# Optimization experiments

Hardware: AMD Instinct MI355X
Metric: run time of the kernel (lower is better)

The kernel has to match this reference:

```python
import jax, jax.numpy as jnp
import numpy as np

N = 50000      # num_nodes
E = 800000     # num_edges
D = 128        # node feature dim
ED = 64        # edge feature dim
H = 4          # num_heads
U = 32         # units per head (units*heads == 128)


def setup_inputs() -> dict:
    key = jax.random.key(0)
    ks = jax.random.split(key, 12)
    inputs = jax.random.normal(ks[0], (N, D), dtype=jnp.float32)
    # tf.math.segment_* requires sorted segment ids -> sort source row
    src = jnp.sort(jax.random.randint(ks[1], (E,), 0, N, dtype=jnp.int32))
    dst = jax.random.randint(ks[2], (E,), 0, N, dtype=jnp.int32)
    edge_index = jnp.stack([src, dst], axis=0)
    edge_features = jax.random.normal(ks[3], (E, ED), dtype=jnp.float32)
    def glorot(k, shape):
        lim = np.sqrt(6.0 / (shape[0] + shape[1]))
        return jax.random.uniform(k, shape, jnp.float32, -lim, lim)
    HU = H * U
    return {
        "inputs": inputs,
        "edge_index": edge_index,
        "edge_features": edge_features,
        "Wq": glorot(ks[4], (D, HU)), "bq": jnp.zeros((HU,), jnp.float32),
        "Wk": glorot(ks[5], (D, HU)), "bk": jnp.zeros((HU,), jnp.float32),
        "Wv": glorot(ks[6], (D, HU)), "bv": jnp.zeros((HU,), jnp.float32),
        "We": glorot(ks[7], (ED, HU)), "be": jnp.zeros((HU,), jnp.float32),
        "Wo": glorot(ks[8], (HU, U)), "bo": jnp.zeros((U,), jnp.float32),
    }


def _segment_softmax(scores, seg, num_segments):
    # numerically stable segmented softmax over ragged neighborhoods
    seg_max = jax.ops.segment_max(scores, seg, num_segments=num_segments)
    ex = jnp.exp(scores - seg_max[seg])
    seg_sum = jax.ops.segment_sum(ex, seg, num_segments=num_segments)
    return ex / seg_sum[seg]


def reference(inputs, edge_index, edge_features, Wq, bq, Wk, bk, Wv, bv, We, be, Wo, bo):
    n = inputs.shape[0]
    q = (inputs @ Wq + bq).reshape(n, H, U)
    k = (inputs @ Wk + bk).reshape(n, H, U)
    v = (inputs @ Wv + bv).reshape(n, H, U)
    src, dst = edge_index[0], edge_index[1]
    qi = q[src]                      # [E, H, U]
    kj = k[dst]                      # [E, H, U]
    scores = jnp.sum(qi * kj, axis=-1)   # [E, H]
    eh = (edge_features @ We + be).reshape(-1, H, U)
    scores = scores + jnp.sum(eh * kj, axis=-1)
    attn = _segment_softmax(scores, src, n)        # [E, H]
    attended = jax.ops.segment_sum(attn[..., None] * v[dst], src, num_segments=n)
    attended = attended.reshape(n, H * U)
    return jax.nn.relu(attended @ Wo + bo)
```

## Files before the change

kernel.cpp:

```cpp
#include <hip/hip_runtime.h>
#include <math.h>

#define N_NODES 50000
#define N_EDGES 800000
#define D_IN    128
#define ED_IN   64
#define HU      128
#define NH      4
#define UD      32

#define NPB 16

typedef float fx4 __attribute__((ext_vector_type(4)));
typedef short s16x8 __attribute__((ext_vector_type(8)));
typedef float f32x4 __attribute__((ext_vector_type(4)));

static __device__ __forceinline__ unsigned short f2bf(float f) {
  unsigned u = __float_as_uint(f);
  unsigned r = (u + 0x7FFFu + ((u >> 16) & 1u)) >> 16;
  return (unsigned short)r;
}
static __device__ __forceinline__ float bf_lo(unsigned u) {
  return __uint_as_float(u << 16);
}
static __device__ __forceinline__ float bf_hi(unsigned u) {
  return __uint_as_float(u & 0xFFFF0000u);
}
static __device__ __forceinline__ float dot8(float4 a0, float4 a1, uint4 kk) {
  return a0.x * bf_lo(kk.x) + a0.y * bf_hi(kk.x)
       + a0.z * bf_lo(kk.y) + a0.w * bf_hi(kk.y)
       + a1.x * bf_lo(kk.z) + a1.y * bf_hi(kk.z)
       + a1.z * bf_lo(kk.w) + a1.w * bf_hi(kk.w);
}
static __device__ __forceinline__ float4 f4add(float4 a, float4 b) {
  return make_float4(a.x + b.x, a.y + b.y, a.z + b.z, a.w + b.w);
}

__global__ __launch_bounds__(256) void offsets_kernel(
    const int* __restrict__ src, int* __restrict__ off) {
  const int e = blockIdx.x * 256 + threadIdx.x;
  if (e >= N_EDGES) return;
  const int s = src[e];
  const int prev = (e == 0) ? -1 : src[e - 1];
  for (int n = prev + 1; n <= s; ++n) off[n] = e;
  if (e == N_EDGES - 1)
    for (int n = s + 1; n <= N_NODES; ++n) off[n] = N_EDGES;
}

__global__ __launch_bounds__(256) void wepack_kernel(
    const float* __restrict__ We, unsigned short* __restrict__ wf) {
  const int fl = blockIdx.x * 256 + threadIdx.x;
  if (fl >= 16 * 64) return;
  const int f = fl >> 6, lane = fl & 63;
  const int nt = f >> 1, kh = f & 1;
  const int n = nt * 16 + (lane & 15);
  const int kbase = kh * 32 + (lane >> 4) * 8;
#pragma unroll
  for (int j = 0; j < 8; ++j)
    wf[fl * 8 + j] = f2bf(We[(kbase + j) * HU + n]);
}

__global__ __launch_bounds__(128) void qkv_kernel(
    const float* __restrict__ x,
    const float* __restrict__ Wq, const float* __restrict__ bq,
    const float* __restrict__ Wk, const float* __restrict__ bk,
    const float* __restrict__ Wv, const float* __restrict__ bv,
    const float* __restrict__ be,
    float* __restrict__ q, unsigned short* __restrict__ kbf,
    unsigned short* __restrict__ vbf) {
  const int base = blockIdx.x * NPB;
  const int t = threadIdx.x;
  __shared__ float xs[NPB][D_IN];
  for (int j = 0; j < NPB; ++j)
    xs[j][t] = x[(long)(base + j) * D_IN + t];
  __syncthreads();
  float aq[NPB], ak[NPB], av[NPB];
  const float bqt = bq[t] + be[t], bkt = bk[t], bvt = bv[t];
#pragma unroll
  for (int j = 0; j < NPB; ++j) { aq[j] = bqt; ak[j] = bkt; av[j] = bvt; }
  for (int i = 0; i < D_IN; ++i) {
    const float wq = Wq[i * HU + t];
    const float wk = Wk[i * HU + t];
    const float wv = Wv[i * HU + t];
#pragma unroll
    for (int j = 0; j < NPB; ++j) {
      const float xi = xs[j][i];
      aq[j] += xi * wq; ak[j] += xi * wk; av[j] += xi * wv;
    }
  }
#pragma unroll
  for (int j = 0; j < NPB; ++j) {
    const long nn = base + j;
    q[nn * HU + t] = aq[j];
    kbf[nn * HU + t] = f2bf(ak[j]);
    vbf[nn * HU + t] = f2bf(av[j]);
  }
}

__global__ __launch_bounds__(256) void score_kernel(
    const float* __restrict__ ef,
    const int* __restrict__ src, const int* __restrict__ dst,
    const float* __restrict__ q, const unsigned short* __restrict__ kbf,
    const s16x8* __restrict__ wf,
    float* __restrict__ scores) {
  __shared__ __align__(16) float ehs[4][16 * 64];
  const int t = threadIdx.x;
  const int w = t >> 6, l = t & 63;
  const long ebase = (long)blockIdx.x * 64;
  const int e = (int)(ebase + w * 16 + (l >> 2));
  const int s = src[e], d = dst[e];

  const int arow = (int)(ebase + w * 16 + (l & 15));
  const fx4* ap = (const fx4*)(ef + (long)arow * ED_IN + (l >> 4) * 8);
  const fx4 a00 = __builtin_nontemporal_load(ap);
  const fx4 a01 = __builtin_nontemporal_load(ap + 1);
  const fx4 a10 = __builtin_nontemporal_load(ap + 8);
  const fx4 a11 = __builtin_nontemporal_load(ap + 9);
  s16x8 A0, A1;
  A0[0] = (short)f2bf(a00[0]); A0[1] = (short)f2bf(a00[1]);
  A0[2] = (short)f2bf(a00[2]); A0[3] = (short)f2bf(a00[3]);
  A0[4] = (short)f2bf(a01[0]); A0[5] = (short)f2bf(a01[1]);
  A0[6] = (short)f2bf(a01[2]); A0[7] = (short)f2bf(a01[3]);
  A1[0] = (short)f2bf(a10[0]); A1[1] = (short)f2bf(a10[1]);
  A1[2] = (short)f2bf(a10[2]); A1[3] = (short)f2bf(a10[3]);
  A1[4] = (short)f2bf(a11[0]); A1[5] = (short)f2bf(a11[1]);
  A1[6] = (short)f2bf(a11[2]); A1[7] = (short)f2bf(a11[3]);

  float* __restrict__ ehw = ehs[w];
  const int nb = l & 15, gbase = (l >> 4) * 4;
  const int rloc = l >> 2;
  const int hl = (l >> 1) & 1, half = l & 1;
  const int swzr = (rloc & 7) << 4;

#pragma unroll
  for (int ph = 0; ph < 2; ++ph) {
    f32x4 acc[4];
#pragma unroll
    for (int ntl = 0; ntl < 4; ++ntl) acc[ntl] = (f32x4){0.f, 0.f, 0.f, 0.f};
#pragma unroll
    for (int ntl = 0; ntl < 4; ++ntl) {
      const int f = (ph * 4 + ntl) * 2;
      const s16x8 B0 = wf[(f + 0) * 64 + l];
      const s16x8 B1 = wf[(f + 1) * 64 + l];
      acc[ntl] = __builtin_amdgcn_mfma_f32_16x16x32_bf16(A0, B0, acc[ntl], 0, 0, 0);
      acc[ntl] = __builtin_amdgcn_mfma_f32_16x16x32_bf16(A1, B1, acc[ntl], 0, 0, 0);
    }

#pragma unroll
    for (int ntl = 0; ntl < 4; ++ntl) {
#pragma unroll
      for (int r = 0; r < 4; ++r) {
        const int m = gbase + r;
        const int b = (ntl * 16 + nb) * 4;
        ehw[(m * 256 + (b ^ ((m & 7) << 4))) >> 2] = acc[ntl][r];
      }
    }
    asm volatile("s_waitcnt lgkmcnt(0)" ::: "memory");
    __builtin_amdgcn_sched_barrier(0);

    const int h = ph * 2 + hl;
    const char* ehp = (const char*)(ehw + rloc * 64);
    const int cb = (l & 3) * 64;
    const float4 e0 = *(const float4*)(ehp + ((cb + 0)  ^ swzr));
    const float4 e1 = *(const float4*)(ehp + ((cb + 16) ^ swzr));
    const float4 e2 = *(const float4*)(ehp + ((cb + 32) ^ swzr));
    const float4 e3 = *(const float4*)(ehp + ((cb + 48) ^ swzr));

    const float4* qp = (const float4*)(q + (long)s * HU + h * 32 + half * 16);
    const float4 q0 = qp[0], q1 = qp[1], q2 = qp[2], q3 = qp[3];
    const uint4* kp = (const uint4*)((const char*)kbf + (long)d * 256 + h * 64 + half * 32);
    const uint4 k0 = kp[0], k1 = kp[1];

    float p = dot8(f4add(q0, e0), f4add(q1, e1), k0)
            + dot8(f4add(q2, e2), f4add(q3, e3), k1);
    p += __shfl_xor(p, 1, 64);
    if (!half)
      __builtin_nontemporal_store(p, scores + (long)e * NH + h);

    asm volatile("s_waitcnt lgkmcnt(0)" ::: "memory");
    __builtin_amdgcn_sched_barrier(0);
  }
}

__global__ __launch_bounds__(256) void aggregate_kernel(
    const int* __restrict__ off, const int* __restrict__ dst,
    const float* __restrict__ scores, const unsigned* __restrict__ v2,
    const float* __restrict__ Wo, const float* __restrict__ bo,
    float* __restrict__ out) {
  const int wv = threadIdx.x >> 6, l = threadIdx.x & 63;
  const int n = blockIdx.x * 4 + wv;
  const int h = l >> 4, q16 = l & 15;
  __shared__ float att[4][HU];

  const int start = off[n], end = off[n + 1];
  float m = -INFINITY, lsum = 0.f, a0 = 0.f, a1 = 0.f;
  for (int cs = start; cs < end; cs += 16) {
    const int e = cs + q16;
    const bool live = (e < end);
    const float sc = live ? __builtin_nontemporal_load(scores + (long)e * NH + h)
                          : -INFINITY;
    const int dl = live ? dst[e] : 0;
    float mc = sc;
#pragma unroll
    for (int o = 8; o > 0; o >>= 1) mc = fmaxf(mc, __shfl_xor(mc, o, 16));
    const float nm = fmaxf(m, mc);
    const float corr = __expf(m - nm);
    const float w = __expf(sc - nm);
    float ws = w;
#pragma unroll
    for (int o = 8; o > 0; o >>= 1) ws += __shfl_xor(ws, o, 16);
    lsum = lsum * corr + ws;
    a0 *= corr; a1 *= corr; m = nm;
#pragma unroll
    for (int j = 0; j < 16; ++j) {
      const float wj = __shfl(w, (l & 48) + j, 64);
      const int dj = __shfl(dl, (l & 48) + j, 64);
      const unsigned vr = v2[(long)dj * 64 + l];
      a0 += wj * bf_lo(vr);
      a1 += wj * bf_hi(vr);
    }
  }
  const float inv = (lsum > 0.f) ? 1.f / lsum : 0.f;
  att[wv][2 * l] = a0 * inv;
  att[wv][2 * l + 1] = a1 * inv;
  const int o = l & 31, half = l >> 5;
  float po = 0.f;
#pragma unroll
  for (int f = 0; f < 64; ++f)
    po += att[wv][half * 64 + f] * Wo[(half * 64 + f) * UD + o];
  po += __shfl_down(po, 32, 64);
  if (l < 32) out[(long)n * UD + l] = fmaxf(po + bo[l], 0.f);
}

extern "C" void kernel_launch(void* const* d_in, const int* in_sizes, int n_in,
                              void* d_out, int out_size, void* d_ws, size_t ws_size,
                              hipStream_t stream) {
  const float* x  = (const float*)d_in[0];
  const int*   ei = (const int*)d_in[1];
  const float* ef = (const float*)d_in[2];
  const float* Wq = (const float*)d_in[3];
  const float* bq = (const float*)d_in[4];
  const float* Wk = (const float*)d_in[5];
  const float* bk = (const float*)d_in[6];
  const float* Wv = (const float*)d_in[7];
  const float* bv = (const float*)d_in[8];
  const float* We = (const float*)d_in[9];
  const float* be = (const float*)d_in[10];
  const float* Wo = (const float*)d_in[11];
  const float* bo = (const float*)d_in[12];
  float* out = (float*)d_out;

  const int* src = ei;
  const int* dst = ei + N_EDGES;

  float* q = (float*)d_ws;
  unsigned short* kbf = (unsigned short*)(q + (long)N_NODES * HU);
  unsigned short* vbf = kbf + (long)N_NODES * HU;
  float* scores = (float*)(vbf + (long)N_NODES * HU);
  int* off = (int*)(scores + (long)N_EDGES * NH);
  unsigned short* wf = (unsigned short*)(((uintptr_t)(off + N_NODES + 1) + 15)
                                         & ~(uintptr_t)15);

  offsets_kernel<<<(N_EDGES + 255) / 256, 256, 0, stream>>>(src, off);
  wepack_kernel<<<4, 256, 0, stream>>>(We, wf);
  qkv_kernel<<<N_NODES / NPB, 128, 0, stream>>>(x, Wq, bq, Wk, bk, Wv, bv, be,
                                                q, kbf, vbf);
  score_kernel<<<N_EDGES / 64, 256, 0, stream>>>(ef, src, dst, q, kbf,
                                                 (const s16x8*)wf, scores);
  aggregate_kernel<<<N_NODES / 4, 256, 0, stream>>>(off, dst, scores,
                                                    (const unsigned*)vbf, Wo, bo, out);
}
```

Before: 493.6 us.

## Use split-bf16 MFMA for QKV projection and stage Wo in LDS

```diff
diff --git a/kernel.cpp b/kernel.cpp
--- a/kernel.cpp
+++ b/kernel.cpp
@@ -9,8 +9,6 @@
 #define NH      4
 #define UD      32
 
-#define NPB 16
-
 typedef float fx4 __attribute__((ext_vector_type(4)));
 typedef short s16x8 __attribute__((ext_vector_type(8)));
 typedef float f32x4 __attribute__((ext_vector_type(4)));
@@ -25,6 +23,9 @@
 }
 static __device__ __forceinline__ float bf_hi(unsigned u) {
   return __uint_as_float(u & 0xFFFF0000u);
+}
+static __device__ __forceinline__ float bf2f(unsigned short h) {
+  return __uint_as_float(((unsigned)h) << 16);
 }
 static __device__ __forceinline__ float dot8(float4 a0, float4 a1, uint4 kk) {
   return a0.x * bf_lo(kk.x) + a0.y * bf_hi(kk.x)
@@ -60,40 +61,77 @@
     wf[fl * 8 + j] = f2bf(We[(kbase + j) * HU + n]);
 }
 
-__global__ __launch_bounds__(128) void qkv_kernel(
-    const float* __restrict__ x,
-    const float* __restrict__ Wq, const float* __restrict__ bq,
-    const float* __restrict__ Wk, const float* __restrict__ bk,
-    const float* __restrict__ Wv, const float* __restrict__ bv,
-    const float* __restrict__ be,
+__global__ __launch_bounds__(256) void wqkvpack_kernel(
+    const float* __restrict__ Wq, const float* __restrict__ Wk,
+    const float* __restrict__ Wv, unsigned short* __restrict__ wqkv) {
+  const int fl = blockIdx.x * 256 + threadIdx.x;
+  if (fl >= 96 * 64) return;
+  const int f = fl >> 6, lane = fl & 63;
+  const int proj = f >> 5, nt = (f >> 2) & 7, kf = f & 3;
+  const float* W = proj == 0 ? Wq : (proj == 1 ? Wk : Wv);
+  const int n = nt * 16 + (lane & 15);
+  const int kb = kf * 32 + (lane >> 4) * 8;
+#pragma unroll
+  for (int j = 0; j < 8; ++j) {
+    const float v = W[(kb + j) * HU + n];
+    const unsigned short h = f2bf(v);
+    wqkv[fl * 8 + j] = h;
+    wqkv[96 * 64 * 8 + fl * 8 + j] = f2bf(v - bf2f(h));
+  }
+}
+
+__global__ __launch_bounds__(256) void qkv_kernel(
+    const float* __restrict__ x, const s16x8* __restrict__ wqkv,
+    const float* __restrict__ bq, const float* __restrict__ be,
+    const float* __restrict__ bk, const float* __restrict__ bv,
     float* __restrict__ q, unsigned short* __restrict__ kbf,
     unsigned short* __restrict__ vbf) {
-  const int base = blockIdx.x * NPB;
+  const int base = blockIdx.x * 16;
   const int t = threadIdx.x;
-  __shared__ float xs[NPB][D_IN];
-  for (int j = 0; j < NPB; ++j)
-    xs[j][t] = x[(long)(base + j) * D_IN + t];
-  __syncthreads();
-  float aq[NPB], ak[NPB], av[NPB];
-  const float bqt = bq[t] + be[t], bkt = bk[t], bvt = bv[t];
-#pragma unroll
-  for (int j = 0; j < NPB; ++j) { aq[j] = bqt; ak[j] = bkt; av[j] = bvt; }
-  for (int i = 0; i < D_IN; ++i) {
-    const float wq = Wq[i * HU + t];
-    const float wk = Wk[i * HU + t];
-    const float wv = Wv[i * HU + t];
-#pragma unroll
-    for (int j = 0; j < NPB; ++j) {
-      const float xi = xs[j][i];
-      aq[j] += xi * wq; ak[j] += xi * wk; av[j] += xi * wv;
-    }
-  }
-#pragma unroll
-  for (int j = 0; j < NPB; ++j) {
-    const long nn = base + j;
-    q[nn * HU + t] = aq[j];
-    kbf[nn * HU + t] = f2bf(ak[j]);
-    vbf[nn * HU + t] = f2bf(av[j]);
+  const int w = t >> 6, l = t & 63;
+
+  const float* xr = x + (long)(base + (l & 15)) * D_IN + (l >> 4) * 8;
+  s16x8 Ah[4], Al[4];
+#pragma unroll
+  for (int kf = 0; kf < 4; ++kf) {
+    const fx4 c0 = *(const fx4*)(xr + kf * 32);
+    const fx4 c1 = *(const fx4*)(xr + kf * 32 + 4);
+#pragma unroll
+    for (int j = 0; j < 4; ++j) {
+      const unsigned short h0 = f2bf(c0[j]);
+      const unsigned short h1 = f2bf(c1[j]);
+      Ah[kf][j] = (short)h0;     Al[kf][j] = (short)f2bf(c0[j] - bf2f(h0));
+      Ah[kf][4 + j] = (short)h1; Al[kf][4 + j] = (short)f2bf(c1[j] - bf2f(h1));
+    }
+  }
+
+#pragma unroll
+  for (int i = 0; i < 6; ++i) {
+    const int tt = w * 6 + i;
+    const int proj = tt >> 3, nt = tt & 7;
+    const int col = nt * 16 + (l & 15);
+    f32x4 acc = (f32x4){0.f, 0.f, 0.f, 0.f};
+#pragma unroll
+    for (int kf = 0; kf < 4; ++kf) {
+      const int fr = proj * 32 + nt * 4 + kf;
+      const s16x8 Bh = wqkv[fr * 64 + l];
+      const s16x8 Bl = wqkv[96 * 64 + fr * 64 + l];
+      acc = __builtin_amdgcn_mfma_f32_16x16x32_bf16(Ah[kf], Bh, acc, 0, 0, 0);
+      acc = __builtin_amdgcn_mfma_f32_16x16x32_bf16(Al[kf], Bh, acc, 0, 0, 0);
+      acc = __builtin_amdgcn_mfma_f32_16x16x32_bf16(Ah[kf], Bl, acc, 0, 0, 0);
+    }
+    float bias;
+    if (proj == 0)      bias = bq[col] + be[col];
+    else if (proj == 1) bias = bk[col];
+    else                bias = bv[col];
+#pragma unroll
+    for (int r = 0; r < 4; ++r) {
+      const long node = base + (l >> 4) * 4 + r;
+      const float val = acc[r] + bias;
+      if (proj == 0)      q[node * HU + col] = val;
+      else if (proj == 1) kbf[node * HU + col] = f2bf(val);
+      else                vbf[node * HU + col] = f2bf(val);
+    }
   }
 }
 
@@ -191,6 +229,16 @@
   const int n = blockIdx.x * 4 + wv;
   const int h = l >> 4, q16 = l & 15;
   __shared__ float att[4][HU];
+  __shared__ __align__(16) float wos[HU * UD];
+
+  {
+    const fx4* wop = (const fx4*)Wo;
+    fx4* wosp = (fx4*)wos;
+#pragma unroll
+    for (int r = 0; r < 4; ++r)
+      wosp[threadIdx.x + 256 * r] = wop[threadIdx.x + 256 * r];
+  }
+  __syncthreads();
 
   const int start = off[n], end = off[n + 1];
   float m = -INFINITY, lsum = 0.f, a0 = 0.f, a1 = 0.f;
@@ -214,7 +262,7 @@
 #pragma unroll
     for (int j = 0; j < 16; ++j) {
       const float wj = __shfl(w, (l & 48) + j, 64);
-      const int dj = __shfl(dl, (l & 48) + j, 64);
+      const int dj = __builtin_amdgcn_readlane(dl, j);
       const unsigned vr = v2[(long)dj * 64 + l];
       a0 += wj * bf_lo(vr);
       a1 += wj * bf_hi(vr);
@@ -227,7 +275,7 @@
   float po = 0.f;
 #pragma unroll
   for (int f = 0; f < 64; ++f)
-    po += att[wv][half * 64 + f] * Wo[(half * 64 + f) * UD + o];
+    po += att[wv][half * 64 + f] * wos[(half * 64 + f) * UD + o];
   po += __shfl_down(po, 32, 64);
   if (l < 32) out[(long)n * UD + l] = fmaxf(po + bo[l], 0.f);
 }
@@ -260,11 +308,13 @@
   int* off = (int*)(scores + (long)N_EDGES * NH);
   unsigned short* wf = (unsigned short*)(((uintptr_t)(off + N_NODES + 1) + 15)
                                          & ~(uintptr_t)15);
+  unsigned short* wqkv = wf + 16 * 64 * 8;
 
   offsets_kernel<<<(N_EDGES + 255) / 256, 256, 0, stream>>>(src, off);
   wepack_kernel<<<4, 256, 0, stream>>>(We, wf);
-  qkv_kernel<<<N_NODES / NPB, 128, 0, stream>>>(x, Wq, bq, Wk, bk, Wv, bv, be,
-                                                q, kbf, vbf);
+  wqkvpack_kernel<<<24, 256, 0, stream>>>(Wq, Wk, Wv, wqkv);
+  qkv_kernel<<<N_NODES / 16, 256, 0, stream>>>(x, (const s16x8*)wqkv,
+                                               bq, be, bk, bv, q, kbf, vbf);
   score_kernel<<<N_EDGES / 64, 256, 0, stream>>>(ef, src, dst, q, kbf,
                                                  (const s16x8*)wf, scores);
   aggregate_kernel<<<N_NODES / 4, 256, 0, stream>>>(off, dst, scores,
```

Measured after the change: 459.2 us. 1.08x faster.
